# Optimization experiments

Measured on AMD Instinct MI355X. Metric: run time of the kernel, lower is better.

## Reference

```python
import jax, jax.numpy as jnp
import numpy as np

B, S, L, H = 8, 4, 512, 768
N_SPANS, T_MAX = 4096, 16
N_PAIRS = 16384


def setup_inputs() -> dict:
    key = jax.random.key(0)
    k1, k2, k3, k4, k5, k6 = jax.random.split(key, 6)
    hidden = jax.random.normal(k1, (B, S, L, H), dtype=jnp.float32)
    span_doc = jax.random.randint(k2, (N_SPANS,), 0, B, dtype=jnp.int32)
    # per-span padded, sorted subtoken indices into the flattened S*L window axis
    span_tok = jnp.sort(jax.random.randint(k3, (N_SPANS, T_MAX), 0, S * L, dtype=jnp.int32), axis=1)
    span_len = jax.random.randint(k4, (N_SPANS,), 1, T_MAX + 1, dtype=jnp.int32)
    pair_i = jax.random.randint(k5, (N_PAIRS,), 0, N_SPANS, dtype=jnp.int32)
    pair_j = jax.random.randint(k6, (N_PAIRS,), 0, N_SPANS, dtype=jnp.int32)
    return {"hidden": hidden, "span_doc": span_doc, "span_tok": span_tok,
            "span_len": span_len, "pair_i": pair_i, "pair_j": pair_j}


def reference(hidden, span_doc, span_tok, span_len, pair_i, pair_j):
    # hidden: [B, S, L, H]; flatten windows so span_tok indexes S*L directly
    b, s, l, h = hidden.shape
    hf = hidden.reshape(b, s * l, h)
    # ragged gather: [N, T, H]
    g = hf[span_doc[:, None], span_tok]
    n, t = span_tok.shape
    mask = (jnp.arange(t, dtype=jnp.int32)[None, :] < span_len[:, None])  # [N, T]
    denom = span_len.astype(hidden.dtype)[:, None]
    mean = jnp.sum(g * mask[..., None].astype(hidden.dtype), axis=1) / denom  # [N, H]
    first = g[:, 0]                                      # first subtoken of span
    last = g[jnp.arange(n), span_len - 1]                # last valid subtoken
    reprs = jnp.concatenate([first, mean, last], axis=-1)  # [N, 3H]
    pairs = jnp.concatenate([reprs[pair_i], reprs[pair_j]], axis=-1)  # [P, 6H]
    return pairs
```

## Files before the change

kernel.cpp:

```cpp
#include <hip/hip_runtime.h>


#define SPAN_HF4  192
#define SPAN_TMAX 16
#define SPAN_SL   2048
#define REPR_F4   576
#define OUT_F4    1152

__global__ __launch_bounds__(192)
void span_reprs_kernel(
    const float4* __restrict__ hidden,
    const int*    __restrict__ span_doc,
    const int*    __restrict__ span_tok,
    const int*    __restrict__ span_len,
    float4*       __restrict__ reprs)
{
    const int s = blockIdx.x;
    const int c = threadIdx.x;

    const int doc = span_doc[s];
    const int len = span_len[s];
    const int* toks = span_tok + s * SPAN_TMAX;
    const float4* base = hidden + (size_t)doc * (SPAN_SL * SPAN_HF4);

    float4 first = make_float4(0.f, 0.f, 0.f, 0.f);
    float4 last  = make_float4(0.f, 0.f, 0.f, 0.f);
    float sx = 0.f, sy = 0.f, sz = 0.f, sw = 0.f;

    #pragma unroll
    for (int t = 0; t < SPAN_TMAX; ++t) {
        const int tc = (t < len) ? t : (len - 1);
        const float4 v = base[(size_t)toks[tc] * SPAN_HF4 + c];
        if (t == 0) first = v;
        last = v;
        const float m = (t < len) ? 1.f : 0.f;
        sx += v.x * m; sy += v.y * m; sz += v.z * m; sw += v.w * m;
    }

    const float inv = 1.0f / (float)len;
    float4* r = reprs + (size_t)s * REPR_F4;
    r[c]       = first;
    r[SPAN_HF4 + c] = make_float4(sx * inv, sy * inv, sz * inv, sw * inv);
    r[2 * SPAN_HF4 + c] = last;
}

__global__ __launch_bounds__(192)
void span_pairs_kernel(
    const float4* __restrict__ reprs,
    const int*    __restrict__ pair_i,
    const int*    __restrict__ pair_j,
    float4*       __restrict__ out,
    int n_pairs)
{
    const int c = threadIdx.x;
    for (int p = blockIdx.x; p < n_pairs; p += gridDim.x) {
        const int pi = pair_i[p];
        const int pj = pair_j[p];
        const float4* ri = reprs + (size_t)pi * REPR_F4;
        const float4* rj = reprs + (size_t)pj * REPR_F4;
        float4* o = out + (size_t)p * OUT_F4;

        const float4 a0 = ri[c];
        const float4 a1 = ri[SPAN_HF4 + c];
        const float4 a2 = ri[2 * SPAN_HF4 + c];
        const float4 b0 = rj[c];
        const float4 b1 = rj[SPAN_HF4 + c];
        const float4 b2 = rj[2 * SPAN_HF4 + c];
        o[c]                 = a0;
        o[SPAN_HF4 + c]      = a1;
        o[2 * SPAN_HF4 + c]  = a2;
        o[3 * SPAN_HF4 + c]  = b0;
        o[4 * SPAN_HF4 + c]  = b1;
        o[5 * SPAN_HF4 + c]  = b2;
    }
}

__global__ __launch_bounds__(192)
void span_fused_kernel(
    const float4* __restrict__ hidden,
    const int*    __restrict__ span_doc,
    const int*    __restrict__ span_tok,
    const int*    __restrict__ span_len,
    const int*    __restrict__ pair_i,
    const int*    __restrict__ pair_j,
    float4*       __restrict__ out)
{
    const int p = blockIdx.x;
    const int c = threadIdx.x;
    const int si = pair_i[p];
    const int sj = pair_j[p];
    float4* orow = out + (size_t)p * OUT_F4;

    #pragma unroll
    for (int side = 0; side < 2; ++side) {
        const int s   = side ? sj : si;
        const int doc = span_doc[s];
        const int len = span_len[s];
        const int* toks = span_tok + s * SPAN_TMAX;
        const float4* base = hidden + (size_t)doc * (SPAN_SL * SPAN_HF4);

        float4 first = make_float4(0.f, 0.f, 0.f, 0.f);
        float4 last  = make_float4(0.f, 0.f, 0.f, 0.f);
        float sx = 0.f, sy = 0.f, sz = 0.f, sw = 0.f;
        #pragma unroll
        for (int t = 0; t < SPAN_TMAX; ++t) {
            const int tc = (t < len) ? t : (len - 1);
            const float4 v = base[(size_t)toks[tc] * SPAN_HF4 + c];
            if (t == 0) first = v;
            last = v;
            const float m = (t < len) ? 1.f : 0.f;
            sx += v.x * m; sy += v.y * m; sz += v.z * m; sw += v.w * m;
        }
        const float inv = 1.0f / (float)len;
        float4* o = orow + side * REPR_F4;
        o[c]                = first;
        o[SPAN_HF4 + c]     = make_float4(sx * inv, sy * inv, sz * inv, sw * inv);
        o[2 * SPAN_HF4 + c] = last;
    }
}

extern "C" void kernel_launch(void* const* d_in, const int* in_sizes, int n_in,
                              void* d_out, int out_size, void* d_ws, size_t ws_size,
                              hipStream_t stream) {
    const float4* hidden  = (const float4*)d_in[0];
    const int* span_doc   = (const int*)d_in[1];
    const int* span_tok   = (const int*)d_in[2];
    const int* span_len   = (const int*)d_in[3];
    const int* pair_i     = (const int*)d_in[4];
    const int* pair_j     = (const int*)d_in[5];
    float4* out           = (float4*)d_out;

    const int n_spans = in_sizes[1];
    const int n_pairs = in_sizes[4];
    const size_t reprs_bytes = (size_t)n_spans * REPR_F4 * sizeof(float4);

    if (ws_size >= reprs_bytes) {
        float4* reprs = (float4*)d_ws;
        span_reprs_kernel<<<n_spans, 192, 0, stream>>>(
            hidden, span_doc, span_tok, span_len, reprs);
        span_pairs_kernel<<<4096, 192, 0, stream>>>(
            reprs, pair_i, pair_j, out, n_pairs);
    } else {
        span_fused_kernel<<<n_pairs, 192, 0, stream>>>(
            hidden, span_doc, span_tok, span_len, pair_i, pair_j, out);
    }
}
```

Before: 390.7 us.

## Scatter span representations directly to pair outputs via inverted index

Replaces the two-stage reprs-then-gather path with a counting sort (count uses, scan offsets, fill targets) that builds, for each span, the list of output slots that reference it. Each span block then computes its representation once and writes it straight into every pair slot that uses it, using nontemporal stores. This removes the intermediate reprs buffer write and its re-read. The cost is four small extra launches with atomics and a serial single-block scan. Load balance may also suffer, since the number of writes per span block varies.

```diff
diff --git a/kernel.cpp b/kernel.cpp
--- a/kernel.cpp
+++ b/kernel.cpp
@@ -6,14 +6,90 @@
 #define SPAN_SL   2048
 #define REPR_F4   576
 #define OUT_F4    1152
+#define MAX_SPANS 4096
+
+typedef float f4nt __attribute__((ext_vector_type(4)));
+
+__device__ __forceinline__ void nt_store_f4(const float4 v, float4* p) {
+    f4nt t;
+    t.x = v.x; t.y = v.y; t.z = v.z; t.w = v.w;
+    __builtin_nontemporal_store(t, reinterpret_cast<f4nt*>(p));
+}
+
+
+__global__ void zero_counts_kernel(int* __restrict__ counts, int n) {
+    const int i = blockIdx.x * blockDim.x + threadIdx.x;
+    if (i < n) counts[i] = 0;
+}
+
+__global__ void count_uses_kernel(const int* __restrict__ pair_i,
+                                  const int* __restrict__ pair_j,
+                                  int* __restrict__ counts, int n_pairs) {
+    const int p = blockIdx.x * blockDim.x + threadIdx.x;
+    if (p < n_pairs) {
+        atomicAdd(&counts[pair_i[p]], 1);
+        atomicAdd(&counts[pair_j[p]], 1);
+    }
+}
+
+__global__ __launch_bounds__(1024)
+void scan_offsets_kernel(const int* __restrict__ counts,
+                         int* __restrict__ offsets,
+                         int* __restrict__ cursor,
+                         int n_spans) {
+    __shared__ int sums[1024];
+    const int t = threadIdx.x;
+    const int base = t * 4;
+    int c0 = 0, c1 = 0, c2 = 0, c3 = 0;
+    if (base     < n_spans) c0 = counts[base];
+    if (base + 1 < n_spans) c1 = counts[base + 1];
+    if (base + 2 < n_spans) c2 = counts[base + 2];
+    if (base + 3 < n_spans) c3 = counts[base + 3];
+    const int local = c0 + c1 + c2 + c3;
+    sums[t] = local;
+    __syncthreads();
+    for (int off = 1; off < 1024; off <<= 1) {
+        const int v = (t >= off) ? sums[t - off] : 0;
+        __syncthreads();
+        sums[t] += v;
+        __syncthreads();
+    }
+    const int excl = (t == 0) ? 0 : sums[t - 1];
+    const int o0 = excl;
+    const int o1 = o0 + c0;
+    const int o2 = o1 + c1;
+    const int o3 = o2 + c2;
+    if (base     < n_spans) { offsets[base]     = o0; cursor[base]     = o0; }
+    if (base + 1 < n_spans) { offsets[base + 1] = o1; cursor[base + 1] = o1; }
+    if (base + 2 < n_spans) { offsets[base + 2] = o2; cursor[base + 2] = o2; }
+    if (base + 3 < n_spans) { offsets[base + 3] = o3; cursor[base + 3] = o3; }
+    if (t == 1023) offsets[n_spans] = sums[1023];
+}
+
+__global__ void fill_targets_kernel(const int* __restrict__ pair_i,
+                                    const int* __restrict__ pair_j,
+                                    int* __restrict__ cursor,
+                                    int* __restrict__ targets,
+                                    int n_pairs) {
+    const int p = blockIdx.x * blockDim.x + threadIdx.x;
+    if (p < n_pairs) {
+        const int a = atomicAdd(&cursor[pair_i[p]], 1);
+        targets[a] = p * 2;
+        const int b = atomicAdd(&cursor[pair_j[p]], 1);
+        targets[b] = p * 2 + 1;
+    }
+}
+
 
 __global__ __launch_bounds__(192)
-void span_reprs_kernel(
+void span_scatter_kernel(
     const float4* __restrict__ hidden,
     const int*    __restrict__ span_doc,
     const int*    __restrict__ span_tok,
     const int*    __restrict__ span_len,
-    float4*       __restrict__ reprs)
+    const int*    __restrict__ offsets,
+    const int*    __restrict__ targets,
+    float4*       __restrict__ out)
 {
     const int s = blockIdx.x;
     const int c = threadIdx.x;
@@ -38,42 +114,29 @@
     }
 
     const float inv = 1.0f / (float)len;
-    float4* r = reprs + (size_t)s * REPR_F4;
-    r[c]       = first;
-    r[SPAN_HF4 + c] = make_float4(sx * inv, sy * inv, sz * inv, sw * inv);
-    r[2 * SPAN_HF4 + c] = last;
-}
-
-__global__ __launch_bounds__(192)
-void span_pairs_kernel(
-    const float4* __restrict__ reprs,
-    const int*    __restrict__ pair_i,
-    const int*    __restrict__ pair_j,
-    float4*       __restrict__ out,
-    int n_pairs)
-{
-    const int c = threadIdx.x;
-    for (int p = blockIdx.x; p < n_pairs; p += gridDim.x) {
-        const int pi = pair_i[p];
-        const int pj = pair_j[p];
-        const float4* ri = reprs + (size_t)pi * REPR_F4;
-        const float4* rj = reprs + (size_t)pj * REPR_F4;
-        float4* o = out + (size_t)p * OUT_F4;
-
-        const float4 a0 = ri[c];
-        const float4 a1 = ri[SPAN_HF4 + c];
-        const float4 a2 = ri[2 * SPAN_HF4 + c];
-        const float4 b0 = rj[c];
-        const float4 b1 = rj[SPAN_HF4 + c];
-        const float4 b2 = rj[2 * SPAN_HF4 + c];
-        o[c]                 = a0;
-        o[SPAN_HF4 + c]      = a1;
-        o[2 * SPAN_HF4 + c]  = a2;
-        o[3 * SPAN_HF4 + c]  = b0;
-        o[4 * SPAN_HF4 + c]  = b1;
-        o[5 * SPAN_HF4 + c]  = b2;
-    }
-}
+    const float4 a0 = first;
+    const float4 a1 = make_float4(sx * inv, sy * inv, sz * inv, sw * inv);
+    const float4 a2 = last;
+
+    __shared__ int tgt[192];
+    const int start = offsets[s];
+    const int end   = offsets[s + 1];
+    for (int cb = start; cb < end; cb += 192) {
+        const int n = min(192, end - cb);
+        if (c < n) tgt[c] = targets[cb + c];
+        __syncthreads();
+        for (int k = 0; k < n; ++k) {
+            const int tv = tgt[k];
+            float4* o = out + (size_t)(tv >> 1) * OUT_F4
+                            + (size_t)(tv & 1) * REPR_F4;
+            nt_store_f4(a0, &o[c]);
+            nt_store_f4(a1, &o[SPAN_HF4 + c]);
+            nt_store_f4(a2, &o[2 * SPAN_HF4 + c]);
+        }
+        __syncthreads();
+    }
+}
+
 
 __global__ __launch_bounds__(192)
 void span_fused_kernel(
@@ -113,11 +176,13 @@
         }
         const float inv = 1.0f / (float)len;
         float4* o = orow + side * REPR_F4;
-        o[c]                = first;
-        o[SPAN_HF4 + c]     = make_float4(sx * inv, sy * inv, sz * inv, sw * inv);
-        o[2 * SPAN_HF4 + c] = last;
-    }
-}
+        nt_store_f4(first, &o[c]);
+        nt_store_f4(make_float4(sx * inv, sy * inv, sz * inv, sw * inv),
+                    &o[SPAN_HF4 + c]);
+        nt_store_f4(last, &o[2 * SPAN_HF4 + c]);
+    }
+}
+
 
 extern "C" void kernel_launch(void* const* d_in, const int* in_sizes, int n_in,
                               void* d_out, int out_size, void* d_ws, size_t ws_size,
@@ -132,14 +197,29 @@
 
     const int n_spans = in_sizes[1];
     const int n_pairs = in_sizes[4];
-    const size_t reprs_bytes = (size_t)n_spans * REPR_F4 * sizeof(float4);
-
-    if (ws_size >= reprs_bytes) {
-        float4* reprs = (float4*)d_ws;
-        span_reprs_kernel<<<n_spans, 192, 0, stream>>>(
-            hidden, span_doc, span_tok, span_len, reprs);
-        span_pairs_kernel<<<4096, 192, 0, stream>>>(
-            reprs, pair_i, pair_j, out, n_pairs);
+
+    auto align16 = [](size_t x) { return (x + 15) & ~(size_t)15; };
+    const size_t counts_b  = align16((size_t)n_spans * sizeof(int));
+    const size_t offsets_b = align16((size_t)(n_spans + 1) * sizeof(int));
+    const size_t cursor_b  = align16((size_t)n_spans * sizeof(int));
+    const size_t targets_b = align16((size_t)2 * n_pairs * sizeof(int));
+    const size_t need = counts_b + offsets_b + cursor_b + targets_b;
+
+    if (n_spans <= MAX_SPANS && ws_size >= need) {
+        char* ws = (char*)d_ws;
+        int* counts  = (int*)(ws);
+        int* offsets = (int*)(ws + counts_b);
+        int* cursor  = (int*)(ws + counts_b + offsets_b);
+        int* targets = (int*)(ws + counts_b + offsets_b + cursor_b);
+
+        const int zb = (n_spans + 255) / 256;
+        const int pb = (n_pairs + 255) / 256;
+        zero_counts_kernel<<<zb, 256, 0, stream>>>(counts, n_spans);
+        count_uses_kernel<<<pb, 256, 0, stream>>>(pair_i, pair_j, counts, n_pairs);
+        scan_offsets_kernel<<<1, 1024, 0, stream>>>(counts, offsets, cursor, n_spans);
+        fill_targets_kernel<<<pb, 256, 0, stream>>>(pair_i, pair_j, cursor, targets, n_pairs);
+        span_scatter_kernel<<<n_spans, 192, 0, stream>>>(
+            hidden, span_doc, span_tok, span_len, offsets, targets, out);
     } else {
         span_fused_kernel<<<n_pairs, 192, 0, stream>>>(
             hidden, span_doc, span_tok, span_len, pair_i, pair_j, out);
```

After: 365.3 us. 1.07x faster.
